# Performance work log

Measured on AMD Instinct MI355X. Metric: run time of the kernel, lower is better.

The kernel has to match this reference:

```python
import jax, jax.numpy as jnp
import numpy as np

B, C, H, W = 8, 256, 64, 64
GROUPS = 32
EPS = 1e-6


def setup_inputs() -> dict:
    key = jax.random.key(0)
    ks = jax.random.split(key, 8)
    s = 0.02
    return {
        "x": jax.random.normal(ks[0], (B, C, H, W), dtype=jnp.float32),
        "gn_scale": jnp.ones((C,), jnp.float32),
        "gn_bias": jnp.zeros((C,), jnp.float32),
        "wq": jax.random.normal(ks[1], (C, C), jnp.float32) * s,
        "bq": jnp.zeros((C,), jnp.float32),
        "wk": jax.random.normal(ks[2], (C, C), jnp.float32) * s,
        "bk": jnp.zeros((C,), jnp.float32),
        "wv": jax.random.normal(ks[3], (C, C), jnp.float32) * s,
        "bv": jnp.zeros((C,), jnp.float32),
        "wproj": jax.random.normal(ks[4], (C, C), jnp.float32) * s,
        "bproj": jnp.zeros((C,), jnp.float32),
    }


def _group_norm(x, scale, bias):
    b, c, h, w = x.shape
    xg = x.reshape(b, GROUPS, c // GROUPS, h, w)
    mean = xg.mean(axis=(2, 3, 4), keepdims=True)
    var = xg.var(axis=(2, 3, 4), keepdims=True)
    xn = ((xg - mean) * jax.lax.rsqrt(var + EPS)).reshape(b, c, h, w)
    return xn * scale[None, :, None, None] + bias[None, :, None, None]


def _conv1x1(x, w, b):
    # 1x1 conv == channel-mixing matmul: w is [out_ch, in_ch]
    return jnp.einsum("oc,bchw->bohw", w, x) + b[None, :, None, None]


def reference(x, gn_scale, gn_bias, wq, bq, wk, bk, wv, bv, wproj, bproj):
    b, c, h, w = x.shape
    hn = _group_norm(x, gn_scale, gn_bias)
    q = _conv1x1(hn, wq, bq).reshape(b, c, h * w)  # [b,c,n]
    k = _conv1x1(hn, wk, bk).reshape(b, c, h * w)
    v = _conv1x1(hn, wv, bv).reshape(b, c, h * w)
    # scores[b,n,m] = <q[:, :, n], k[:, :, m]> * c^-0.5  (softmax over keys m)
    scale = jnp.asarray(c, x.dtype) ** -0.5
    attn = jax.nn.softmax(jnp.einsum("bcn,bcm->bnm", q, k) * scale, axis=2)
    # h_[b,c,n] = sum_m v[b,c,m] * attn[b,n,m]
    h_ = jnp.einsum("bcm,bnm->bcn", v, attn).reshape(b, c, h, w)
    h_ = _conv1x1(h_, wproj, bproj)
    return x + h_
```

## Files before the change

kernel.cpp:

```cpp
#include <hip/hip_runtime.h>

#define B_ 8
#define C_ 256
#define N_ 4096
#define G_ 32

typedef __bf16 bf16;
typedef __bf16 bf16x8 __attribute__((ext_vector_type(8)));
typedef float f32x4 __attribute__((ext_vector_type(4)));
typedef float f32x16 __attribute__((ext_vector_type(16)));
typedef long i64;
typedef long i64x2 __attribute__((ext_vector_type(2)));
typedef long i64x2a __attribute__((ext_vector_type(2), may_alias));
typedef int i32x8 __attribute__((ext_vector_type(8)));
typedef int i32x8a __attribute__((ext_vector_type(8), may_alias));
typedef unsigned int u32;
typedef unsigned char u8;
typedef unsigned short u16;
typedef unsigned long long u64;

__device__ __forceinline__ f32x4 mfma16(bf16x8 a, bf16x8 b, f32x4 c) {
    return __builtin_amdgcn_mfma_f32_16x16x32_bf16(a, b, c, 0, 0, 0);
}
__device__ __forceinline__ f32x16 mfma_mx(i32x8 a, i32x8 b, f32x16 c) {
    return __builtin_amdgcn_mfma_scale_f32_32x32x64_f8f6f4(
        a, b, c, 0 , 0 , 0, 0x7F7F7F7F, 0, 0x7F7F7F7F);
}

typedef __attribute__((address_space(1))) const void* gas_t;
typedef __attribute__((address_space(3))) void* las_t;
__device__ __forceinline__ void gl2lds16(const void* g, void* l) {
    __builtin_amdgcn_global_load_lds((gas_t)g, (las_t)l, 16, 0, 0);
}

__device__ __forceinline__ float exp2_hw(float x) {
    return __builtin_amdgcn_exp2f(x);
}

__device__ __forceinline__ u32 fp8_fast(float x) {
    union { float f; u32 u; } c;
    c.f = x;
    return ((c.u + 0x00080000u) >> 20) - 960u;
}
__device__ __forceinline__ u32 pk_fp8x4(float a, float b, float c, float d) {
#if __has_builtin(__builtin_amdgcn_cvt_pk_fp8_f32)
    int w = __builtin_amdgcn_cvt_pk_fp8_f32(a, b, 0, false);
    w = __builtin_amdgcn_cvt_pk_fp8_f32(c, d, w, true);
    return (u32)w;
#else
    return (fp8_fast(a) & 0xff) | ((fp8_fast(b) & 0xff) << 8) |
           ((fp8_fast(c) & 0xff) << 16) | (fp8_fast(d) << 24);
#endif
}

__global__ __launch_bounds__(256) void gn_part(const float* __restrict__ x,
                                               float* __restrict__ gpart) {
    int blk = blockIdx.x;
    int b = blk >> 8, g = (blk >> 3) & 31, qe = blk & 7;
    int tid = threadIdx.x;
    int c = g * 8 + (tid >> 5);
    const float* row = x + ((size_t)(b * C_ + c)) * N_ + qe * 512;
    float s = 0.f, s2 = 0.f;
    for (int n = (tid & 31) * 4; n < 512; n += 128) {
        float4 v = *(const float4*)(row + n);
        s += v.x + v.y + v.z + v.w;
        s2 += v.x * v.x + v.y * v.y + v.z * v.z + v.w * v.w;
    }
    for (int off = 32; off; off >>= 1) {
        s += __shfl_xor(s, off);
        s2 += __shfl_xor(s2, off);
    }
    __shared__ float red[8];
    int wid = tid >> 6;
    if ((tid & 63) == 0) { red[wid] = s; red[4 + wid] = s2; }
    __syncthreads();
    if (tid == 0) {
        gpart[blk * 2] = red[0] + red[1] + red[2] + red[3];
        gpart[blk * 2 + 1] = red[4] + red[5] + red[6] + red[7];
    }
}

__global__ __launch_bounds__(256) void gn_apply(const float* __restrict__ x,
                                                const float* __restrict__ gsc,
                                                const float* __restrict__ gbi,
                                                const float* __restrict__ gpart,
                                                bf16* __restrict__ hn) {
    __shared__ float tile[32][33];
    int b = blockIdx.z, c0 = blockIdx.y * 32, n0 = blockIdx.x * 32;
    int tx = threadIdx.x & 31, ty = threadIdx.x >> 5;
    for (int i = 0; i < 4; i++) {
        int cl = ty + i * 8;
        int c = c0 + cl;
        int g = c >> 3;
        const float* gp = gpart + ((size_t)(b * G_ + g)) * 16;
        float S = 0.f, S2 = 0.f;
#pragma unroll
        for (int j = 0; j < 8; j++) { S += gp[j * 2]; S2 += gp[j * 2 + 1]; }
        float mean = S * (1.f / 32768.f);
        float var = S2 * (1.f / 32768.f) - mean * mean;
        float rstd = rsqrtf(var + 1e-6f);
        float sc = gsc[c] * rstd;
        float bs = gbi[c] - mean * sc;
        float v = x[((size_t)(b * C_ + c)) * N_ + n0 + tx];
        tile[cl][tx] = v * sc + bs;
    }
    __syncthreads();
    for (int i = 0; i < 4; i++) {
        int nl = ty + i * 8;
        hn[((size_t)(b * N_ + n0 + nl)) * C_ + c0 + tx] = (bf16)tile[tx][nl];
    }
}

__global__ __launch_bounds__(256) void cvt_w(const float* __restrict__ wq,
                                             const float* __restrict__ wk,
                                             const float* __restrict__ wv,
                                             const float* __restrict__ wp,
                                             bf16* __restrict__ dst) {
    int i = blockIdx.x * 256 + threadIdx.x;
    dst[i] = (bf16)wq[i];
    dst[65536 + i] = (bf16)wk[i];
    dst[131072 + i] = (bf16)wv[i];
    dst[196608 + i] = (bf16)wp[i];
}

__global__ __launch_bounds__(256) void gemm_qkv(const bf16* __restrict__ A,
                                                const bf16* __restrict__ Wq,
                                                const bf16* __restrict__ Wk,
                                                const bf16* __restrict__ Wv,
                                                const float* __restrict__ bq,
                                                const float* __restrict__ bk,
                                                const float* __restrict__ bv,
                                                u8* __restrict__ q8,
                                                u8* __restrict__ k8,
                                                u8* __restrict__ v8) {
    __shared__ __align__(16) bf16 As[64][32];
    __shared__ __align__(16) bf16 Wqs[64][32];
    __shared__ __align__(16) bf16 Wks[64][32];
    __shared__ __align__(16) bf16 Wvs[64][32];
    int m0 = blockIdx.x * 64;
    int n0 = blockIdx.y * 64;
    int tid = threadIdx.x;
    int wv_ = tid >> 6, lane = tid & 63, lr = lane & 15, lq = lane >> 4;
    int wm = (wv_ & 1) * 32, wn = (wv_ >> 1) * 32;
    int sr = tid >> 2, sk = (tid & 3) * 8;
    f32x4 qacc[2][2] = {}, kacc[2][2] = {}, vacc[2][2] = {};
    for (int kk = 0; kk < C_; kk += 32) {
        __syncthreads();
        gl2lds16(&A[(size_t)(m0 + sr) * C_ + kk + sk], &As[sr][sk]);
        gl2lds16(&Wq[(size_t)(n0 + sr) * C_ + kk + sk], &Wqs[sr][sk]);
        gl2lds16(&Wk[(size_t)(n0 + sr) * C_ + kk + sk], &Wks[sr][sk]);
        gl2lds16(&Wv[(size_t)(n0 + sr) * C_ + kk + sk], &Wvs[sr][sk]);
        __syncthreads();
        bf16x8 a0 = *(const bf16x8*)&As[wm + lr][lq * 8];
        bf16x8 a1 = *(const bf16x8*)&As[wm + 16 + lr][lq * 8];
        bf16x8 q0 = *(const bf16x8*)&Wqs[wn + lr][lq * 8];
        bf16x8 q1 = *(const bf16x8*)&Wqs[wn + 16 + lr][lq * 8];
        bf16x8 k0 = *(const bf16x8*)&Wks[wn + lr][lq * 8];
        bf16x8 k1 = *(const bf16x8*)&Wks[wn + 16 + lr][lq * 8];
        bf16x8 v0 = *(const bf16x8*)&Wvs[wn + lr][lq * 8];
        bf16x8 v1 = *(const bf16x8*)&Wvs[wn + 16 + lr][lq * 8];
        qacc[0][0] = mfma16(a0, q0, qacc[0][0]);
        qacc[0][1] = mfma16(a0, q1, qacc[0][1]);
        qacc[1][0] = mfma16(a1, q0, qacc[1][0]);
        qacc[1][1] = mfma16(a1, q1, qacc[1][1]);
        kacc[0][0] = mfma16(a0, k0, kacc[0][0]);
        kacc[0][1] = mfma16(a0, k1, kacc[0][1]);
        kacc[1][0] = mfma16(a1, k0, kacc[1][0]);
        kacc[1][1] = mfma16(a1, k1, kacc[1][1]);
        vacc[0][0] = mfma16(a0, v0, vacc[0][0]);
        vacc[0][1] = mfma16(a0, v1, vacc[0][1]);
        vacc[1][0] = mfma16(a1, v0, vacc[1][0]);
        vacc[1][1] = mfma16(a1, v1, vacc[1][1]);
    }
    for (int i = 0; i < 2; i++)
        for (int j = 0; j < 2; j++) {
            int col = n0 + wn + j * 16 + lr;
            float bvq = bq[col], bvk = bk[col], bvv = bv[col];
            u32 qw = pk_fp8x4(qacc[i][j][0] + bvq, qacc[i][j][1] + bvq,
                              qacc[i][j][2] + bvq, qacc[i][j][3] + bvq);
            u32 kw = pk_fp8x4(kacc[i][j][0] + bvk, kacc[i][j][1] + bvk,
                              kacc[i][j][2] + bvk, kacc[i][j][3] + bvk);
            u32 vw = pk_fp8x4(vacc[i][j][0] + bvv, vacc[i][j][1] + bvv,
                              vacc[i][j][2] + bvv, vacc[i][j][3] + bvv);
            for (int r = 0; r < 4; r++) {
                int row = m0 + wm + i * 16 + lq * 4 + r;
                q8[(size_t)row * C_ + col] = (u8)(qw >> (8 * r));
                k8[(size_t)row * C_ + col] = (u8)(kw >> (8 * r));
                int bb = row >> 12, n = row & (N_ - 1);
                int h = (n >> 11) & 1, mtl = (n >> 6) & 31, k6 = n & 63;
                int hbv = (k6 >> 2) & 1;
                int jv = ((k6 >> 5) << 4) | (((k6 >> 3) & 3) << 2) | (k6 & 3);
                jv ^= ((col ^ hbv) & 1) << 4;
                v8[((size_t)(((bb * 2 + h) * 32 + mtl) * 2 + hbv)) * 8192 +
                   col * 32 + jv] = (u8)(vw >> (8 * r));
            }
        }
}

__global__ __launch_bounds__(256, 2) void attn(const u8* __restrict__ q,
                                               const u8* __restrict__ k,
                                               const u8* __restrict__ vT,
                                               bf16* __restrict__ O0,
                                               bf16* __restrict__ O1,
                                               float* __restrict__ lp) {
    __shared__ __align__(16) u8 smem[65536];

    int flat = blockIdx.x;
    int nid = (flat & 7) * 64 + (flat >> 3);
    int q0 = (nid & 31) * 128;
    int h = (nid >> 5) & 1;
    int b = nid >> 6;
    int tid = threadIdx.x;
    int w = tid >> 6, lane = tid & 63, lc = lane & 31, hb = lane >> 5;

    const u8* kglob = k + ((size_t)(b * N_) + h * 2048) * 256;
    const u8* vglob = vT + ((size_t)(b * 2 + h)) * 32 * 16384;

    u32 offK[4], lin[4];
#pragma unroll
    for (int j = 0; j < 4; j++) {
        int p = j * 256 + tid;
        int rK = p >> 4;
        offK[j] = (u32)(rK * 256 + (((p & 15) ^ (rK & 15)) << 4));
        lin[j] = (u32)(p << 4);
    }

    const u8* qrow = q + ((size_t)(b * N_ + q0 + w * 32 + lc)) * 256 + hb * 32;
    i32x8 qf[4];
#pragma unroll
    for (int kh = 0; kh < 4; kh++) qf[kh] = *(const i32x8a*)&qrow[kh * 64];

    f32x16 oacc[8] = {};
    f32x16 eacc = {};
    i32x8 pfA = {};
    u32 swz = (u32)(lc & 15);
    u32 vsw0 = (u32)(((lc ^ hb) & 1) << 4);

    auto STAGE_KP = [&](int mt, u32 koff) {
        const u8* kg = kglob + (size_t)mt * 16384;
#pragma unroll
        for (int j = 0; j < 4; j++) gl2lds16(kg + offK[j], smem + koff + lin[j]);
    };
    auto STAGE_V = [&](int mt, u32 voff) {
        const u8* vg = vglob + (size_t)mt * 16384;
#pragma unroll
        for (int j = 0; j < 4; j++) gl2lds16(vg + lin[j], smem + voff + lin[j]);
    };
    auto QKT = [&](u32 koff, f32x16& st0, f32x16& st1) {
        const u8* Ka = smem + koff;
        const u8* Kb = smem + koff + 8192;
#pragma unroll
        for (int kh = 0; kh < 4; kh++) {
            u32 g0 = (u32)(kh * 4 + hb * 2);
            union { i64x2 h2[2]; i32x8 v; } kf0, kf1;
            kf0.h2[0] = *(const i64x2a*)&Ka[lc * 256 + ((g0 ^ swz) << 4)];
            kf0.h2[1] = *(const i64x2a*)&Ka[lc * 256 + (((g0 + 1) ^ swz) << 4)];
            st0 = mfma_mx(kf0.v, qf[kh], st0);
            kf1.h2[0] = *(const i64x2a*)&Kb[lc * 256 + ((g0 ^ swz) << 4)];
            kf1.h2[1] = *(const i64x2a*)&Kb[lc * 256 + (((g0 + 1) ^ swz) << 4)];
            st1 = mfma_mx(kf1.v, qf[kh], st1);
        }
    };
    auto PV = [&](u32 voff, i32x8 pf) {
#pragma unroll
        for (int ct = 0; ct < 8; ct++) {
            u32 base = voff + (u32)(hb * 8192 + (ct * 32 + lc) * 32);
            union { i64x2 h2[2]; i32x8 v; } vf;
            vf.h2[0] = *(const i64x2a*)&smem[base + vsw0];
            vf.h2[1] = *(const i64x2a*)&smem[base + (vsw0 ^ 16)];
            oacc[ct] = mfma_mx(pf, vf.v, oacc[ct]);
        }
    };
    auto SM = [&](const f32x16& st0, const f32x16& st1) {
        f32x16 e0, e1;
#pragma unroll
        for (int i = 0; i < 16; i++) {
            e0[i] = exp2_hw(st0[i] * (1.44269504089f * 0.0625f));
            e1[i] = exp2_hw(st1[i] * (1.44269504089f * 0.0625f));
        }
        eacc += e0;
        eacc += e1;
#pragma unroll
        for (int t4 = 0; t4 < 4; t4++) {
            pfA[t4] = (int)pk_fp8x4(e0[t4 * 4], e0[t4 * 4 + 1], e0[t4 * 4 + 2],
                                    e0[t4 * 4 + 3]);
            pfA[4 + t4] = (int)pk_fp8x4(e1[t4 * 4], e1[t4 * 4 + 1], e1[t4 * 4 + 2],
                                        e1[t4 * 4 + 3]);
        }
    };

    STAGE_KP(0, 0);
    asm volatile("s_waitcnt vmcnt(0)" ::: "memory");
    __builtin_amdgcn_s_barrier();
    STAGE_KP(1, 16384);
    STAGE_V(0, 32768);
    {
        __builtin_amdgcn_s_setprio(1);
        f32x16 st0 = {}, st1 = {};
        QKT(0, st0, st1);
        SM(st0, st1);
        __builtin_amdgcn_s_setprio(0);
    }
    for (int mt = 1; mt <= 30; ++mt) {
        asm volatile("s_waitcnt vmcnt(0)" ::: "memory");
        __builtin_amdgcn_s_barrier();
        STAGE_KP(mt + 1, (u32)(((mt + 1) & 1) * 16384));
        STAGE_V(mt, (u32)(32768 + (mt & 1) * 16384));
        __builtin_amdgcn_s_setprio(1);
        f32x16 st0 = {}, st1 = {};
        QKT((u32)((mt & 1) * 16384), st0, st1);
        PV((u32)(32768 + ((mt - 1) & 1) * 16384), pfA);
        SM(st0, st1);
        __builtin_amdgcn_s_setprio(0);
    }
    asm volatile("s_waitcnt vmcnt(0)" ::: "memory");
    __builtin_amdgcn_s_barrier();
    STAGE_V(31, 32768 + 16384);
    {
        __builtin_amdgcn_s_setprio(1);
        f32x16 st0 = {}, st1 = {};
        QKT(16384, st0, st1);
        PV(32768, pfA);
        SM(st0, st1);
        __builtin_amdgcn_s_setprio(0);
    }
    asm volatile("s_waitcnt vmcnt(0)" ::: "memory");
    __builtin_amdgcn_s_barrier();
    PV(32768 + 16384, pfA);

    float hs = 0.f;
#pragma unroll
    for (int i = 0; i < 16; i++) hs += eacc[i];
    float lsum = hs + __shfl_xor(hs, 32);

    bf16* Op = h ? O1 : O0;
#pragma unroll
    for (int ct = 0; ct < 8; ct++)
#pragma unroll
        for (int r = 0; r < 16; r++) {
            int qq = (r & 3) + hb * 4 + (r >> 2) * 8;
            Op[((size_t)(b * N_ + q0 + w * 32 + qq)) * C_ + ct * 32 + lc] =
                (bf16)oacc[ct][r];
        }
    if (hb == 0)
        lp[((size_t)(h * B_ + b)) * N_ + q0 + w * 32 + lc] = lsum;
}

__global__ __launch_bounds__(256) void proj_res(const bf16* __restrict__ W,
                                                const bf16* __restrict__ O0,
                                                const bf16* __restrict__ O1,
                                                const float* __restrict__ lp,
                                                const float* __restrict__ bias,
                                                const float* __restrict__ x,
                                                float* __restrict__ out) {
    __shared__ __align__(16) bf16 Ws[256][32];
    __shared__ __align__(16) bf16 As[64][32];
    int n0 = blockIdx.x * 64;
    int tid = threadIdx.x;
    int wv_ = tid >> 6, lane = tid & 63, lr = lane & 15, lq = lane >> 4;
    int wm = (wv_ & 1) * 32;
    int wn = (wv_ >> 1) * 32;
    int sr = tid >> 2, sk = (tid & 3) * 8;
    int T = n0 + sr, bb = T >> 12, nn = T & (N_ - 1);
    float inv = 1.f / (lp[(size_t)bb * N_ + nn] + lp[(size_t)(B_ + bb) * N_ + nn]);
    f32x4 acc[4][2][2] = {};
    for (int kk = 0; kk < C_; kk += 32) {
        __syncthreads();
#pragma unroll
        for (int p = 0; p < 4; p++)
            gl2lds16(&W[(size_t)(p * 64 + sr) * C_ + kk + sk], &Ws[p * 64 + sr][sk]);
        bf16x8 o0 = *(const bf16x8*)&O0[(size_t)T * C_ + kk + sk];
        bf16x8 o1 = *(const bf16x8*)&O1[(size_t)T * C_ + kk + sk];
        bf16x8 cm;
#pragma unroll
        for (int e = 0; e < 8; e++) cm[e] = (bf16)(((float)o0[e] + (float)o1[e]) * inv);
        *(bf16x8*)&As[sr][sk] = cm;
        __syncthreads();
        bf16x8 a0 = *(const bf16x8*)&As[wm + lr][lq * 8];
        bf16x8 a1 = *(const bf16x8*)&As[wm + 16 + lr][lq * 8];
#pragma unroll
        for (int ot = 0; ot < 4; ot++) {
            bf16x8 w0 = *(const bf16x8*)&Ws[ot * 64 + wn + lr][lq * 8];
            bf16x8 w1 = *(const bf16x8*)&Ws[ot * 64 + wn + 16 + lr][lq * 8];
            acc[ot][0][0] = mfma16(w0, a0, acc[ot][0][0]);
            acc[ot][0][1] = mfma16(w0, a1, acc[ot][0][1]);
            acc[ot][1][0] = mfma16(w1, a0, acc[ot][1][0]);
            acc[ot][1][1] = mfma16(w1, a1, acc[ot][1][1]);
        }
    }
#pragma unroll
    for (int ot = 0; ot < 4; ot++)
        for (int i = 0; i < 2; i++)
            for (int j = 0; j < 2; j++) {
                int Tt = n0 + wm + j * 16 + lr;
                int b = Tt >> 12, n = Tt & (N_ - 1);
                for (int r = 0; r < 4; r++) {
                    int o = ot * 64 + wn + i * 16 + lq * 4 + r;
                    size_t idx = ((size_t)(b * C_ + o)) * N_ + n;
                    out[idx] = x[idx] + acc[ot][i][j][r] + bias[o];
                }
            }
}

extern "C" void kernel_launch(void* const* d_in, const int* in_sizes, int n_in,
                              void* d_out, int out_size, void* d_ws, size_t ws_size,
                              hipStream_t stream) {
    const float* x = (const float*)d_in[0];
    const float* gsc = (const float*)d_in[1];
    const float* gbi = (const float*)d_in[2];
    const float* wq = (const float*)d_in[3];
    const float* bq = (const float*)d_in[4];
    const float* wk = (const float*)d_in[5];
    const float* bk = (const float*)d_in[6];
    const float* wv = (const float*)d_in[7];
    const float* bv = (const float*)d_in[8];
    const float* wp = (const float*)d_in[9];
    const float* bp = (const float*)d_in[10];
    float* out = (float*)d_out;

    const size_t SZ = (size_t)B_ * N_ * C_;
    char* ws = (char*)d_ws;
    bf16* wb = (bf16*)(ws + 4096);
    char* base = ws + 4096 + 524288;
    bf16* hn = (bf16*)base;
    u8* q8 = (u8*)(base + SZ * 2);
    u8* k8 = (u8*)(base + SZ * 3);
    u8* v8 = (u8*)(base + SZ * 4);
    bf16* O0 = (bf16*)base;
    bf16* O1 = (bf16*)(base + SZ * 5);
    float* gpart = (float*)(base + SZ * 7);
    float* lpart = (float*)(base + SZ * 7);

    cvt_w<<<256, 256, 0, stream>>>(wq, wk, wv, wp, wb);
    gn_part<<<B_ * G_ * 8, 256, 0, stream>>>(x, gpart);
    gn_apply<<<dim3(N_ / 32, C_ / 32, B_), 256, 0, stream>>>(x, gsc, gbi, gpart, hn);
    gemm_qkv<<<dim3(B_ * N_ / 64, C_ / 64), 256, 0, stream>>>(
        hn, wb, wb + 65536, wb + 131072, bq, bk, bv, q8, k8, v8);
    attn<<<512, 256, 0, stream>>>(q8, k8, v8, O0, O1, lpart);
    proj_res<<<B_ * N_ / 64, 256, 0, stream>>>(
        wb + 196608, O0, O1, lpart, bp, x, out);
}
```

Before: 263.7 us.

## Shrink attention blocks to two waves and restructure K/V staging pipeline

The attention kernel now launches 1024 blocks of 128 threads, each covering 64 queries instead of 128. Shared memory drops to 48KB: one K buffer plus a double-buffered V. The loop is rewritten so the score MFMAs are followed by a barrier, then the next K/V tiles are prefetched while softmax and PV run, with a one-tile lag and a changed swizzle rotation for the K layout. The aim is higher occupancy and more blocks, at the cost of an extra barrier per tile and each K/V tile being read by twice as many blocks.

```diff
diff --git a/kernel.cpp b/kernel.cpp
--- a/kernel.cpp
+++ b/kernel.cpp
@@ -197,31 +197,32 @@
         }
 }
 
-__global__ __launch_bounds__(256, 2) void attn(const u8* __restrict__ q,
+__global__ __launch_bounds__(128, 2) void attn(const u8* __restrict__ q,
                                                const u8* __restrict__ k,
                                                const u8* __restrict__ vT,
                                                bf16* __restrict__ O0,
                                                bf16* __restrict__ O1,
                                                float* __restrict__ lp) {
-    __shared__ __align__(16) u8 smem[65536];
+    __shared__ __align__(16) u8 smem[49152];
 
     int flat = blockIdx.x;
-    int nid = (flat & 7) * 64 + (flat >> 3);
-    int q0 = (nid & 31) * 128;
-    int h = (nid >> 5) & 1;
-    int b = nid >> 6;
+    int nid = (flat & 7) * 128 + (flat >> 3);
+    int q0 = (nid & 63) * 64;
+    int h = (nid >> 6) & 1;
+    int b = nid >> 7;
     int tid = threadIdx.x;
     int w = tid >> 6, lane = tid & 63, lc = lane & 31, hb = lane >> 5;
 
     const u8* kglob = k + ((size_t)(b * N_) + h * 2048) * 256;
     const u8* vglob = vT + ((size_t)(b * 2 + h)) * 32 * 16384;
 
-    u32 offK[4], lin[4];
-#pragma unroll
-    for (int j = 0; j < 4; j++) {
-        int p = j * 256 + tid;
-        int rK = p >> 4;
-        offK[j] = (u32)(rK * 256 + (((p & 15) ^ (rK & 15)) << 4));
+    u32 offK[8], lin[8];
+#pragma unroll
+    for (int j = 0; j < 8; j++) {
+        int p = j * 128 + tid;
+        int rK = p >> 4, r4 = rK & 15;
+        int rot = ((r4 << 1) | (r4 >> 3)) & 15;
+        offK[j] = (u32)(rK * 256 + (((p & 15) ^ rot) << 4));
         lin[j] = (u32)(p << 4);
     }
 
@@ -233,42 +234,43 @@
     f32x16 oacc[8] = {};
     f32x16 eacc = {};
     i32x8 pfA = {};
-    u32 swz = (u32)(lc & 15);
+    int l4 = lc & 15;
+    u32 swzR = (u32)(((l4 << 1) | (l4 >> 3)) & 15);
     u32 vsw0 = (u32)(((lc ^ hb) & 1) << 4);
 
-    auto STAGE_KP = [&](int mt, u32 koff) {
+    auto STAGE_K = [&](int mt) {
         const u8* kg = kglob + (size_t)mt * 16384;
 #pragma unroll
-        for (int j = 0; j < 4; j++) gl2lds16(kg + offK[j], smem + koff + lin[j]);
+        for (int j = 0; j < 8; j++) gl2lds16(kg + offK[j], smem + lin[j]);
     };
     auto STAGE_V = [&](int mt, u32 voff) {
         const u8* vg = vglob + (size_t)mt * 16384;
 #pragma unroll
-        for (int j = 0; j < 4; j++) gl2lds16(vg + lin[j], smem + voff + lin[j]);
+        for (int j = 0; j < 8; j++) gl2lds16(vg + lin[j], smem + voff + lin[j]);
     };
-    auto QKT = [&](u32 koff, f32x16& st0, f32x16& st1) {
-        const u8* Ka = smem + koff;
-        const u8* Kb = smem + koff + 8192;
+    auto QKT = [&](f32x16& st0, f32x16& st1) {
+        const u8* Ka = smem;
+        const u8* Kb = smem + 8192;
 #pragma unroll
         for (int kh = 0; kh < 4; kh++) {
             u32 g0 = (u32)(kh * 4 + hb * 2);
             union { i64x2 h2[2]; i32x8 v; } kf0, kf1;
-            kf0.h2[0] = *(const i64x2a*)&Ka[lc * 256 + ((g0 ^ swz) << 4)];
-            kf0.h2[1] = *(const i64x2a*)&Ka[lc * 256 + (((g0 + 1) ^ swz) << 4)];
+            kf0.h2[0] = *(const i64x2a*)&Ka[lc * 256 + ((g0 ^ swzR) << 4)];
+            kf0.h2[1] = *(const i64x2a*)&Ka[lc * 256 + (((g0 + 1) ^ swzR) << 4)];
             st0 = mfma_mx(kf0.v, qf[kh], st0);
-            kf1.h2[0] = *(const i64x2a*)&Kb[lc * 256 + ((g0 ^ swz) << 4)];
-            kf1.h2[1] = *(const i64x2a*)&Kb[lc * 256 + (((g0 + 1) ^ swz) << 4)];
+            kf1.h2[0] = *(const i64x2a*)&Kb[lc * 256 + ((g0 ^ swzR) << 4)];
+            kf1.h2[1] = *(const i64x2a*)&Kb[lc * 256 + (((g0 + 1) ^ swzR) << 4)];
             st1 = mfma_mx(kf1.v, qf[kh], st1);
         }
     };
-    auto PV = [&](u32 voff, i32x8 pf) {
+    auto PV = [&](u32 voff) {
 #pragma unroll
         for (int ct = 0; ct < 8; ct++) {
             u32 base = voff + (u32)(hb * 8192 + (ct * 32 + lc) * 32);
             union { i64x2 h2[2]; i32x8 v; } vf;
             vf.h2[0] = *(const i64x2a*)&smem[base + vsw0];
             vf.h2[1] = *(const i64x2a*)&smem[base + (vsw0 ^ 16)];
-            oacc[ct] = mfma_mx(pf, vf.v, oacc[ct]);
+            oacc[ct] = mfma_mx(pfA, vf.v, oacc[ct]);
         }
     };
     auto SM = [&](const f32x16& st0, const f32x16& st1) {
@@ -289,44 +291,27 @@
         }
     };
 
-    STAGE_KP(0, 0);
-    asm volatile("s_waitcnt vmcnt(0)" ::: "memory");
-    __builtin_amdgcn_s_barrier();
-    STAGE_KP(1, 16384);
-    STAGE_V(0, 32768);
-    {
+    STAGE_K(0);
+    STAGE_V(0, 16384);
+    for (int mt = 0; mt < 32; ++mt) {
+        asm volatile("s_waitcnt vmcnt(8)" ::: "memory");
+        __builtin_amdgcn_s_barrier();
         __builtin_amdgcn_s_setprio(1);
         f32x16 st0 = {}, st1 = {};
-        QKT(0, st0, st1);
-        SM(st0, st1);
+        QKT(st0, st1);
         __builtin_amdgcn_s_setprio(0);
-    }
-    for (int mt = 1; mt <= 30; ++mt) {
+        asm volatile("s_waitcnt lgkmcnt(0)" ::: "memory");
         asm volatile("s_waitcnt vmcnt(0)" ::: "memory");
         __builtin_amdgcn_s_barrier();
-        STAGE_KP(mt + 1, (u32)(((mt + 1) & 1) * 16384));
-        STAGE_V(mt, (u32)(32768 + (mt & 1) * 16384));
+        if (mt < 31) {
+            STAGE_K(mt + 1);
+            STAGE_V(mt + 1, (u32)(16384 + ((mt + 1) & 1) * 16384));
+        }
         __builtin_amdgcn_s_setprio(1);
-        f32x16 st0 = {}, st1 = {};
-        QKT((u32)((mt & 1) * 16384), st0, st1);
-        PV((u32)(32768 + ((mt - 1) & 1) * 16384), pfA);
         SM(st0, st1);
+        PV((u32)(16384 + (mt & 1) * 16384));
         __builtin_amdgcn_s_setprio(0);
     }
-    asm volatile("s_waitcnt vmcnt(0)" ::: "memory");
-    __builtin_amdgcn_s_barrier();
-    STAGE_V(31, 32768 + 16384);
-    {
-        __builtin_amdgcn_s_setprio(1);
-        f32x16 st0 = {}, st1 = {};
-        QKT(16384, st0, st1);
-        PV(32768, pfA);
-        SM(st0, st1);
-        __builtin_amdgcn_s_setprio(0);
-    }
-    asm volatile("s_waitcnt vmcnt(0)" ::: "memory");
-    __builtin_amdgcn_s_barrier();
-    PV(32768 + 16384, pfA);
 
     float hs = 0.f;
 #pragma unroll
@@ -436,7 +421,7 @@
     gn_apply<<<dim3(N_ / 32, C_ / 32, B_), 256, 0, stream>>>(x, gsc, gbi, gpart, hn);
     gemm_qkv<<<dim3(B_ * N_ / 64, C_ / 64), 256, 0, stream>>>(
         hn, wb, wb + 65536, wb + 131072, bq, bk, bv, q8, k8, v8);
-    attn<<<512, 256, 0, stream>>>(q8, k8, v8, O0, O1, lpart);
+    attn<<<1024, 128, 0, stream>>>(q8, k8, v8, O0, O1, lpart);
     proj_res<<<B_ * N_ / 64, 256, 0, stream>>>(
         wb + 196608, O0, O1, lpart, bp, x, out);
 }
```

After: 275.5 us. +4.5%, slower.
